# Kernel tuning notes

Measured on AMD Instinct MI355X. Metric: run time of the kernel, lower is better.

The kernel has to match this reference:

```python
import jax, jax.numpy as jnp
import numpy as np

B, C, H, W = 16, 64, 128, 128


def setup_inputs() -> dict:
    key = jax.random.key(0)
    k1, k2, k3 = jax.random.split(key, 3)
    return {
        "template_map": jax.random.normal(k1, (B, C, H, W), dtype=jnp.float32),
        "roi_map": jax.random.normal(k2, (B, C, H, W), dtype=jnp.float32),
        "gamma": jnp.zeros((1,), dtype=jnp.float32),
        "omega": jnp.zeros((1,), dtype=jnp.float32),
        "conv_w": jax.random.normal(k3, (C, 2 * C), dtype=jnp.float32) * 0.05,
        "conv_b": jnp.zeros((C,), dtype=jnp.float32),
    }


def _chan_attn(x):
    # x: [B, C, H, W] -> attention over channels [B, C, C] and flat values [B, C, N]
    b, c, h, w = x.shape
    v = x.reshape(b, c, h * w)
    energy = jnp.einsum('bcn,bdn->bcd', v, v)  # [B, C, C]
    energy_new = jnp.max(energy, axis=-1, keepdims=True) - energy
    attn = jax.nn.softmax(energy_new, axis=-1)
    return attn, v


def reference(template_map, roi_map, gamma, omega, conv_w, conv_b):
    b, c, th, tw = template_map.shape
    _, _, rh, rw = roi_map.shape
    t_attn, t_v = _chan_attn(template_map)
    r_attn, r_v = _chan_attn(roi_map)
    # cross application: roi attention reweights template channels, and vice versa
    t_out = jnp.einsum('bcd,bdn->bcn', r_attn, t_v).reshape(b, c, th, tw)
    t_out = gamma * t_out + template_map
    r_out = jnp.einsum('bcd,bdn->bcn', t_attn, r_v).reshape(b, c, rh, rw)
    r_out = omega * r_out + roi_map
    fused = jnp.concatenate([t_out, r_out], axis=1)  # [B, 2C, H, W]
    # 1x1 conv == channel-mixing einsum
    out = jnp.einsum('bchw,oc->bohw', fused, conv_w) + conv_b[None, :, None, None]
    return out
```

## Files before the change

kernel.cpp:

```cpp
#include <hip/hip_runtime.h>

typedef __attribute__((ext_vector_type(8))) short short8;
typedef __attribute__((ext_vector_type(4))) float floatx4;
typedef unsigned int uint;
typedef unsigned short ushort;

#define BATCH 16
#define CH 64
#define NPIX 16384
#define TWOC 128

__device__ __forceinline__ ushort f2bf(float f) {
    uint u = __float_as_uint(f);
    u += 0x7FFFu + ((u >> 16) & 1u);
    return (ushort)(u >> 16);
}
__device__ __forceinline__ uint pk2(float lo, float hi) {
    return (uint)f2bf(lo) | ((uint)f2bf(hi) << 16);
}

typedef const __attribute__((address_space(1))) void gas_void;
typedef __attribute__((address_space(3))) void las_void;
__device__ __forceinline__ void gload16(const void* g, void* l) {
    __builtin_amdgcn_global_load_lds((gas_void*)g, (las_void*)l, 16, 0, 0);
}

__global__ __launch_bounds__(256) void gram_kernel(
    const float* __restrict__ tmap, const float* __restrict__ rmap,
    const float* __restrict__ gamma, const float* __restrict__ omega,
    float* __restrict__ G)
{
    const int map = blockIdx.y;
    const float mult = (map == 0) ? omega[0] : gamma[0];
    if (mult == 0.f) return;

    __shared__ float tile[64][68];
    const int chunk = blockIdx.x;
    const int b     = blockIdx.z;
    const float* x = (map == 0 ? tmap : rmap) + (size_t)b * CH * NPIX + chunk * 512;
    const int t  = threadIdx.x;
    const int ti = t >> 4;
    const int tj = t & 15;

    float acc[4][4];
#pragma unroll
    for (int i = 0; i < 4; ++i)
#pragma unroll
        for (int j = 0; j < 4; ++j) acc[i][j] = 0.f;

    for (int tt = 0; tt < 8; ++tt) {
        const int col0 = tt * 64;
#pragma unroll
        for (int k = 0; k < 16; ++k) {
            int e = t + 256 * k;
            int c = e >> 6, col = e & 63;
            tile[c][col] = x[(size_t)c * NPIX + col0 + col];
        }
        __syncthreads();
#pragma unroll 8
        for (int n = 0; n < 64; n += 2) {
            float2 av[4], bv[4];
#pragma unroll
            for (int i = 0; i < 4; ++i) av[i] = *(const float2*)&tile[ti + 16 * i][n];
#pragma unroll
            for (int j = 0; j < 4; ++j) bv[j] = *(const float2*)&tile[tj + 16 * j][n];
#pragma unroll
            for (int i = 0; i < 4; ++i)
#pragma unroll
                for (int j = 0; j < 4; ++j) {
                    acc[i][j] += av[i].x * bv[j].x;
                    acc[i][j] += av[i].y * bv[j].y;
                }
        }
        __syncthreads();
    }
    float* Gp = G + ((size_t)(b * 2 + map) << 12);
#pragma unroll
    for (int i = 0; i < 4; ++i)
#pragma unroll
        for (int j = 0; j < 4; ++j)
            atomicAdd(&Gp[(ti + 16 * i) * 64 + (tj + 16 * j)], acc[i][j]);
}

__global__ __launch_bounds__(128) void finalize_kernel(
    const float* __restrict__ G, const float* __restrict__ gamma,
    const float* __restrict__ omega, const float* __restrict__ conv_w,
    ushort* __restrict__ Mtf)
{
    __shared__ float attn[2][64][64];
    const int b = blockIdx.x;
    const int t = threadIdx.x;
    const float gam = gamma[0], om = omega[0];
    {
        const int map = t >> 6, i = t & 63;
        const float need = (map == 0) ? om : gam;
        if (need != 0.f) {
            const float* Grow = G + ((size_t)(b * 2 + map) << 12) + i * 64;
            float mn = Grow[0];
            for (int j = 1; j < 64; ++j) mn = fminf(mn, Grow[j]);
            float s = 0.f;
            for (int j = 0; j < 64; ++j) s += expf(mn - Grow[j]);
            const float inv = 1.f / s;
            for (int j = 0; j < 64; ++j) attn[map][i][j] = expf(mn - Grow[j]) * inv;
        }
    }
    __syncthreads();
    for (int idx = t; idx < 8192; idx += 128) {
        const int e     = idx & 7;
        const int l     = (idx >> 3) & 63;
        const int mi    = (idx >> 9) & 3;
        const int kstep = idx >> 11;
        const int row = mi * 16 + (l & 15);
        const int k   = kstep * 32 + (l >> 4) * 8 + e;
        const float* wrow = conv_w + row * TWOC;
        float v = wrow[k];
        if (k < 64) {
            if (gam != 0.f) {
                float dot = 0.f;
                for (int c = 0; c < 64; ++c) dot += wrow[c] * attn[1][c][k];
                v += gam * dot;
            }
        } else {
            const int d = k - 64;
            if (om != 0.f) {
                float dot = 0.f;
                for (int c = 0; c < 64; ++c) dot += wrow[64 + c] * attn[0][c][d];
                v += om * dot;
            }
        }
        Mtf[(size_t)b * 8192 + idx] = f2bf(v);
    }
}

__global__ __launch_bounds__(256, 2) void out_kernel(
    const float* __restrict__ tmap, const float* __restrict__ rmap,
    const ushort* __restrict__ Mtf, const float* __restrict__ conv_b,
    float* __restrict__ out)
{
    __shared__ __align__(16) uint Xs[2][32][256];

    const int b   = blockIdx.y;
    const int t   = threadIdx.x;
    const int w   = t >> 6;
    const int l   = t & 63;
    const int lg  = l >> 4;
    const int lj  = l & 15;
    const int px0 = blockIdx.x * 256;

    const ushort* mbase = Mtf + (size_t)b * 8192;
    const float*  tb = tmap + (size_t)b * CH * NPIX + px0;
    const float*  rb = rmap + (size_t)b * CH * NPIX + px0;

#define SRC(c) (((c) < 2 ? tb : rb) + (size_t)(((c) & 1) * 32) * NPIX)

    short8 a[2][4];
#pragma unroll
    for (int i = 0; i < 8; ++i) {
        const int row = i * 4 + w;
        gload16(SRC(0) + (size_t)row * NPIX + 4 * l, &Xs[0][row][0]);
    }
#pragma unroll
    for (int mi = 0; mi < 4; ++mi)
        a[0][mi] = *(const short8*)&mbase[((0 * 4 + mi) * 64 + l) * 8];
#pragma unroll
    for (int i = 0; i < 8; ++i) {
        const int row = i * 4 + w;
        gload16(SRC(1) + (size_t)row * NPIX + 4 * l, &Xs[1][row][0]);
    }
#pragma unroll
    for (int mi = 0; mi < 4; ++mi)
        a[1][mi] = *(const short8*)&mbase[((1 * 4 + mi) * 64 + l) * 8];

    floatx4 acc[4][4];
#pragma unroll
    for (int mi = 0; mi < 4; ++mi)
#pragma unroll
        for (int nj = 0; nj < 4; ++nj) acc[mi][nj] = (floatx4){0.f, 0.f, 0.f, 0.f};

#pragma unroll
    for (int c = 0; c < 4; ++c) {
        if (c < 3) { asm volatile("s_waitcnt vmcnt(12)" ::: "memory"); }
        else       { asm volatile("s_waitcnt vmcnt(0)"  ::: "memory"); }
        __builtin_amdgcn_sched_barrier(0);
        __builtin_amdgcn_s_barrier();
        __builtin_amdgcn_sched_barrier(0);

#pragma unroll
        for (int nj = 0; nj < 4; ++nj) {
            const int pxl = w * 64 + nj * 16 + lj;
            float v[8];
#pragma unroll
            for (int e = 0; e < 8; ++e)
                v[e] = __uint_as_float(Xs[c & 1][8 * lg + e][pxl]);
            uint4 bu;
            bu.x = pk2(v[0], v[1]);
            bu.y = pk2(v[2], v[3]);
            bu.z = pk2(v[4], v[5]);
            bu.w = pk2(v[6], v[7]);
            const short8 bb = *(const short8*)&bu;
#pragma unroll
            for (int mi = 0; mi < 4; ++mi)
                acc[mi][nj] = __builtin_amdgcn_mfma_f32_16x16x32_bf16(
                    a[c & 1][mi], bb, acc[mi][nj], 0, 0, 0);
        }

        asm volatile("s_waitcnt lgkmcnt(0)" ::: "memory");
        __builtin_amdgcn_sched_barrier(0);
        __builtin_amdgcn_s_barrier();
        __builtin_amdgcn_sched_barrier(0);

        if (c < 2) {
            const int cn = c + 2;
#pragma unroll
            for (int i = 0; i < 8; ++i) {
                const int row = i * 4 + w;
                gload16(SRC(cn) + (size_t)row * NPIX + 4 * l, &Xs[c & 1][row][0]);
            }
#pragma unroll
            for (int mi = 0; mi < 4; ++mi)
                a[c & 1][mi] = *(const short8*)&mbase[((cn * 4 + mi) * 64 + l) * 8];
        }
    }
#undef SRC

    const int pxw = px0 + w * 64;
#pragma unroll
    for (int mi = 0; mi < 4; ++mi) {
#pragma unroll
        for (int r = 0; r < 4; ++r) {
            const int och = mi * 16 + lg * 4 + r;
            const float bv = conv_b[och];
            float* orow = out + ((size_t)b * CH + och) * NPIX;
#pragma unroll
            for (int nj = 0; nj < 4; ++nj)
                orow[pxw + nj * 16 + lj] = acc[mi][nj][r] + bv;
        }
    }
}

extern "C" void kernel_launch(void* const* d_in, const int* in_sizes, int n_in,
                              void* d_out, int out_size, void* d_ws, size_t ws_size,
                              hipStream_t stream) {
    const float* tmap   = (const float*)d_in[0];
    const float* rmap   = (const float*)d_in[1];
    const float* gamma  = (const float*)d_in[2];
    const float* omega  = (const float*)d_in[3];
    const float* conv_w = (const float*)d_in[4];
    const float* conv_b = (const float*)d_in[5];
    float* out = (float*)d_out;

    float*  G   = (float*)d_ws;
    ushort* Mtf = (ushort*)((char*)d_ws + (size_t)BATCH * 2 * 4096 * sizeof(float));

    hipMemsetAsync(d_ws, 0, (size_t)BATCH * 2 * 4096 * sizeof(float), stream);

    gram_kernel<<<dim3(32, 2, BATCH), 256, 0, stream>>>(tmap, rmap, gamma, omega, G);
    finalize_kernel<<<dim3(BATCH), 128, 0, stream>>>(G, gamma, omega, conv_w, Mtf);
    out_kernel<<<dim3(64, BATCH), 256, 0, stream>>>(tmap, rmap, Mtf, conv_b, out);
}
```

Measured before the change: 55.75 us.

## Fuse finalize kernel into output kernel, building mixing matrix in LDS per block

The separate finalize kernel, which built the per-batch bf16 mixing matrix from the Gram matrices and conv weights, is removed. Each output block now recomputes that matrix into shared memory, taking a cheap conversion-only path when gamma and omega are zero, and keeps all four A-fragment sets in registers. This drops one kernel launch and a global round trip for the matrix. The cost is redundant per-block recomputation when the attention path is active, plus extra LDS and registers that may lower occupancy.

```diff
diff --git a/kernel.cpp b/kernel.cpp
--- a/kernel.cpp
+++ b/kernel.cpp
@@ -82,62 +82,14 @@
             atomicAdd(&Gp[(ti + 16 * i) * 64 + (tj + 16 * j)], acc[i][j]);
 }
 
-__global__ __launch_bounds__(128) void finalize_kernel(
+__global__ __launch_bounds__(256, 2) void out_kernel(
+    const float* __restrict__ tmap, const float* __restrict__ rmap,
     const float* __restrict__ G, const float* __restrict__ gamma,
     const float* __restrict__ omega, const float* __restrict__ conv_w,
-    ushort* __restrict__ Mtf)
+    const float* __restrict__ conv_b, float* __restrict__ out)
 {
-    __shared__ float attn[2][64][64];
-    const int b = blockIdx.x;
-    const int t = threadIdx.x;
-    const float gam = gamma[0], om = omega[0];
-    {
-        const int map = t >> 6, i = t & 63;
-        const float need = (map == 0) ? om : gam;
-        if (need != 0.f) {
-            const float* Grow = G + ((size_t)(b * 2 + map) << 12) + i * 64;
-            float mn = Grow[0];
-            for (int j = 1; j < 64; ++j) mn = fminf(mn, Grow[j]);
-            float s = 0.f;
-            for (int j = 0; j < 64; ++j) s += expf(mn - Grow[j]);
-            const float inv = 1.f / s;
-            for (int j = 0; j < 64; ++j) attn[map][i][j] = expf(mn - Grow[j]) * inv;
-        }
-    }
-    __syncthreads();
-    for (int idx = t; idx < 8192; idx += 128) {
-        const int e     = idx & 7;
-        const int l     = (idx >> 3) & 63;
-        const int mi    = (idx >> 9) & 3;
-        const int kstep = idx >> 11;
-        const int row = mi * 16 + (l & 15);
-        const int k   = kstep * 32 + (l >> 4) * 8 + e;
-        const float* wrow = conv_w + row * TWOC;
-        float v = wrow[k];
-        if (k < 64) {
-            if (gam != 0.f) {
-                float dot = 0.f;
-                for (int c = 0; c < 64; ++c) dot += wrow[c] * attn[1][c][k];
-                v += gam * dot;
-            }
-        } else {
-            const int d = k - 64;
-            if (om != 0.f) {
-                float dot = 0.f;
-                for (int c = 0; c < 64; ++c) dot += wrow[64 + c] * attn[0][c][d];
-                v += om * dot;
-            }
-        }
-        Mtf[(size_t)b * 8192 + idx] = f2bf(v);
-    }
-}
-
-__global__ __launch_bounds__(256, 2) void out_kernel(
-    const float* __restrict__ tmap, const float* __restrict__ rmap,
-    const ushort* __restrict__ Mtf, const float* __restrict__ conv_b,
-    float* __restrict__ out)
-{
-    __shared__ __align__(16) uint Xs[2][32][256];
+    __shared__ __align__(16) uint   Xs[2][32][256];
+    __shared__ __align__(16) ushort Ms[8192];
 
     const int b   = blockIdx.y;
     const int t   = threadIdx.x;
@@ -147,40 +99,98 @@
     const int lj  = l & 15;
     const int px0 = blockIdx.x * 256;
 
-    const ushort* mbase = Mtf + (size_t)b * 8192;
-    const float*  tb = tmap + (size_t)b * CH * NPIX + px0;
-    const float*  rb = rmap + (size_t)b * CH * NPIX + px0;
-
+    const float gam = gamma[0], om = omega[0];
+
+    if (gam != 0.f || om != 0.f) {
+        float* attnf = (float*)&Xs[0][0][0];
+        if (t < 128) {
+            const int map = t >> 6, i = t & 63;
+            const float need = (map == 0) ? om : gam;
+            if (need != 0.f) {
+                const float* Grow = G + ((size_t)(b * 2 + map) << 12) + i * 64;
+                float mn = Grow[0];
+                for (int j = 1; j < 64; ++j) mn = fminf(mn, Grow[j]);
+                float s = 0.f;
+                for (int j = 0; j < 64; ++j) s += expf(mn - Grow[j]);
+                const float inv = 1.f / s;
+                for (int j = 0; j < 64; ++j)
+                    attnf[(map << 12) + i * 64 + j] = expf(mn - Grow[j]) * inv;
+            }
+        }
+        __syncthreads();
+#pragma unroll
+        for (int j = 0; j < 32; ++j) {
+            const int idx = t + 256 * j;
+            const int e = idx & 7, ll = (idx >> 3) & 63;
+            const int mi = (idx >> 9) & 3, kstep = idx >> 11;
+            const int row = mi * 16 + (ll & 15);
+            const int k   = kstep * 32 + (ll >> 4) * 8 + e;
+            const float* wrow = conv_w + row * TWOC;
+            float v = wrow[k];
+            if (k < 64) {
+                if (gam != 0.f) {
+                    float dot = 0.f;
+                    for (int c = 0; c < 64; ++c) dot += wrow[c] * attnf[(1 << 12) + c * 64 + k];
+                    v += gam * dot;
+                }
+            } else {
+                if (om != 0.f) {
+                    float dot = 0.f;
+                    for (int c = 0; c < 64; ++c) dot += wrow[64 + c] * attnf[c * 64 + (k - 64)];
+                    v += om * dot;
+                }
+            }
+            Ms[idx] = f2bf(v);
+        }
+        __syncthreads();
+    } else {
+#pragma unroll
+        for (int j = 0; j < 32; ++j) {
+            const int idx = t + 256 * j;
+            const int e = idx & 7, ll = (idx >> 3) & 63;
+            const int mi = (idx >> 9) & 3, kstep = idx >> 11;
+            const int row = mi * 16 + (ll & 15);
+            const int k   = kstep * 32 + (ll >> 4) * 8 + e;
+            Ms[idx] = f2bf(conv_w[row * TWOC + k]);
+        }
+    }
+
+    const float* tb = tmap + (size_t)b * CH * NPIX + px0;
+    const float* rb = rmap + (size_t)b * CH * NPIX + px0;
 #define SRC(c) (((c) < 2 ? tb : rb) + (size_t)(((c) & 1) * 32) * NPIX)
 
-    short8 a[2][4];
 #pragma unroll
     for (int i = 0; i < 8; ++i) {
         const int row = i * 4 + w;
         gload16(SRC(0) + (size_t)row * NPIX + 4 * l, &Xs[0][row][0]);
     }
 #pragma unroll
-    for (int mi = 0; mi < 4; ++mi)
-        a[0][mi] = *(const short8*)&mbase[((0 * 4 + mi) * 64 + l) * 8];
-#pragma unroll
     for (int i = 0; i < 8; ++i) {
         const int row = i * 4 + w;
         gload16(SRC(1) + (size_t)row * NPIX + 4 * l, &Xs[1][row][0]);
     }
+
+    asm volatile("s_waitcnt lgkmcnt(0)" ::: "memory");
+    __builtin_amdgcn_s_barrier();
+    __builtin_amdgcn_sched_barrier(0);
+
+    short8 a[4][4];
+#pragma unroll
+    for (int c = 0; c < 4; ++c)
+#pragma unroll
+        for (int mi = 0; mi < 4; ++mi)
+            a[c][mi] = *(const short8*)&Ms[((c * 4 + mi) * 64 + l) * 8];
+
+    floatx4 acc[4][4];
 #pragma unroll
     for (int mi = 0; mi < 4; ++mi)
-        a[1][mi] = *(const short8*)&mbase[((1 * 4 + mi) * 64 + l) * 8];
-
-    floatx4 acc[4][4];
-#pragma unroll
-    for (int mi = 0; mi < 4; ++mi)
 #pragma unroll
         for (int nj = 0; nj < 4; ++nj) acc[mi][nj] = (floatx4){0.f, 0.f, 0.f, 0.f};
 
 #pragma unroll
     for (int c = 0; c < 4; ++c) {
-        if (c < 3) { asm volatile("s_waitcnt vmcnt(12)" ::: "memory"); }
-        else       { asm volatile("s_waitcnt vmcnt(0)"  ::: "memory"); }
+        if (c < 3) { asm volatile("s_waitcnt vmcnt(8) lgkmcnt(0)" ::: "memory"); }
+        else       { asm volatile("s_waitcnt vmcnt(0) lgkmcnt(0)" ::: "memory"); }
         __builtin_amdgcn_sched_barrier(0);
         __builtin_amdgcn_s_barrier();
         __builtin_amdgcn_sched_barrier(0);
@@ -201,7 +211,7 @@
 #pragma unroll
             for (int mi = 0; mi < 4; ++mi)
                 acc[mi][nj] = __builtin_amdgcn_mfma_f32_16x16x32_bf16(
-                    a[c & 1][mi], bb, acc[mi][nj], 0, 0, 0);
+                    a[c][mi], bb, acc[mi][nj], 0, 0, 0);
         }
 
         asm volatile("s_waitcnt lgkmcnt(0)" ::: "memory");
@@ -216,9 +226,6 @@
                 const int row = i * 4 + w;
                 gload16(SRC(cn) + (size_t)row * NPIX + 4 * l, &Xs[c & 1][row][0]);
             }
-#pragma unroll
-            for (int mi = 0; mi < 4; ++mi)
-                a[c & 1][mi] = *(const short8*)&mbase[((cn * 4 + mi) * 64 + l) * 8];
         }
     }
 #undef SRC
@@ -249,12 +256,11 @@
     const float* conv_b = (const float*)d_in[5];
     float* out = (float*)d_out;
 
-    float*  G   = (float*)d_ws;
-    ushort* Mtf = (ushort*)((char*)d_ws + (size_t)BATCH * 2 * 4096 * sizeof(float));
+    float* G = (float*)d_ws;
 
     hipMemsetAsync(d_ws, 0, (size_t)BATCH * 2 * 4096 * sizeof(float), stream);
 
     gram_kernel<<<dim3(32, 2, BATCH), 256, 0, stream>>>(tmap, rmap, gamma, omega, G);
-    finalize_kernel<<<dim3(BATCH), 128, 0, stream>>>(G, gamma, omega, conv_w, Mtf);
-    out_kernel<<<dim3(64, BATCH), 256, 0, stream>>>(tmap, rmap, Mtf, conv_b, out);
-}
+    out_kernel<<<dim3(64, BATCH), 256, 0, stream>>>(tmap, rmap, G, gamma, omega,
+                                                    conv_w, conv_b, out);
+}
```

After: 45.49 us, median of 2. -18.4%, faster.
